# Optimization experiments

Hardware: AMD Instinct MI355X
Metric: run time of the kernel (lower is better)

The kernel has to match this reference:

```python
import jax, jax.numpy as jnp
import numpy as np

V, NLAB, NLAYERS, DI, DM, DS, DD, K = 32000, 9, 2, 768, 1536, 16, 96, 4
B, S = 2, 2048
EPS = 1e-6


def setup_inputs() -> dict:
    key = jax.random.key(0)
    ks = jax.random.split(key, 12)
    n = lambda k, shape, s=0.02: jax.random.normal(k, shape, jnp.float32) * s
    return {
        "input_ids": jax.random.randint(ks[0], (B, S), 0, V, dtype=jnp.int32),
        "attention_mask": jnp.ones((B, S), jnp.int32),
        "emb": n(ks[1], (V, DI)),
        "norm_w": jnp.ones((NLAYERS, DI), jnp.float32),
        "in_proj_w": n(ks[2], (NLAYERS, 2 * DM, DI)),
        "conv_w": n(ks[3], (NLAYERS, DM, K), 0.1),
        "conv_b": jnp.zeros((NLAYERS, DM), jnp.float32),
        "sB_w": n(ks[4], (NLAYERS, DS, DM)),
        "sC_w": n(ks[5], (NLAYERS, DS, DM)),
        "sD1_w": n(ks[6], (NLAYERS, DD, DM)),
        "sD2_w": n(ks[7], (NLAYERS, DM, DD)),
        "A": jnp.tile(jnp.arange(1, DS + 1, dtype=jnp.float32), (NLAYERS, DM, 1)),
        "Dp": jnp.ones((NLAYERS, DM), jnp.float32),
        "out_w": n(ks[8], (NLAYERS, DI, DM)),
        "cls_w": n(ks[9], (NLAB, DI)),
        "cls_b": jnp.zeros((NLAB,), jnp.float32),
    }


def _rmsnorm(x, w):
    return x * jax.lax.rsqrt(jnp.mean(x * x, axis=-1, keepdims=True) + EPS) * w


def _mamba_block(x, norm_w, Wi, cw, cb, WB, WC, W1, W2, A, Dp, Wo):
    # x: (b, l, d_input)
    h = _rmsnorm(x, norm_w)
    a, gate = jnp.split(h @ Wi.T, 2, axis=-1)  # each (b, l, DM)
    # causal depthwise conv1d, kernel K, left-pad K-1 (== Conv1d(pad=K-1)[..., :l])
    L = a.shape[1]
    ap = jnp.pad(a, ((0, 0), (K - 1, 0), (0, 0)))
    conv = cb + sum(ap[:, i:i + L, :] * cw[:, i] for i in range(K))
    a = jax.nn.silu(conv)
    # selective SSM
    Bm = a @ WB.T                                   # (b, l, DS)
    Cm = a @ WC.T                                   # (b, l, DS)
    delta = jax.nn.softplus(Dp + (a @ W1.T) @ W2.T)  # (b, l, DM)
    A_bar = jnp.exp(delta[..., None] * (-A))         # (b, l, DM, DS)
    X_bar = (delta * a)[..., None] * Bm[:, :, None, :]  # (b, l, DM, DS)

    def comb(c1, c2):
        a1, x1 = c1
        a2, x2 = c2
        return a1 * a2, a2 * x1 + x2

    _, hid = jax.lax.associative_scan(comb, (A_bar, X_bar), axis=1)
    y = jnp.einsum('blds,bls->bld', hid, Cm) + Dp * a
    y = y * jax.nn.silu(gate)
    return y @ Wo.T


def _forward(input_ids, attention_mask, emb, norm_w, in_proj_w, conv_w, conv_b,
             sB_w, sC_w, sD1_w, sD2_w, A, Dp, out_w, cls_w, cls_b):
    x = emb[input_ids] * attention_mask[..., None].astype(emb.dtype)
    for i in range(NLAYERS):  # residual Mamba layers
        x = _mamba_block(x, norm_w[i], in_proj_w[i], conv_w[i], conv_b[i],
                         sB_w[i], sC_w[i], sD1_w[i], sD2_w[i], A[i], Dp[i], out_w[i]) + x
    # dropout is identity at inference
    return x @ cls_w.T + cls_b  # logits (b, l, num_labels)


def reference(input_ids, attention_mask, emb, norm_w, in_proj_w, conv_w, conv_b,
              sB_w, sC_w, sD1_w, sD2_w, A, Dp, out_w, cls_w, cls_b):
    return _forward(input_ids, attention_mask, emb, norm_w, in_proj_w, conv_w, conv_b,
                    sB_w, sC_w, sD1_w, sD2_w, A, Dp, out_w, cls_w, cls_b)
```

## Files before the change

kernel.cpp:

```cpp
#include <hip/hip_runtime.h>
#include <hip/hip_bf16.h>
#include <math.h>

#define NLAB 9
#define NL   2
#define DI   768
#define DM   1536
#define DS   16
#define KC   4
#define DD   96
#define BB   2
#define SS   2048
#define TT   (BB*SS)
#define EPSF 1e-6f

#define NCH  64
#define CL   (SS/NCH)

#define NW   128
#define KS   8
#define KSL  (DM/KS)

typedef __attribute__((ext_vector_type(4))) float f32x4;
typedef __attribute__((ext_vector_type(8))) short bf16x8;
typedef __attribute__((ext_vector_type(4))) unsigned short us4;

__device__ __forceinline__ float siluf(float x) { return x / (1.f + __expf(-x)); }
__device__ __forceinline__ float softplusf(float x) { return x > 15.f ? x : log1pf(__expf(x)); }

__device__ __forceinline__ unsigned short f2bf(float f) {
    unsigned u = __float_as_uint(f);
    return (unsigned short)((u + 0x7fffu + ((u >> 16) & 1u)) >> 16);
}

__global__ void f32_to_bf16(const float* __restrict__ src,
                            unsigned short* __restrict__ dst, int n)
{
    int i = (blockIdx.x * 256 + threadIdx.x) * 8;
    if (i >= n) return;
    float4 a = *(const float4*)(src + i);
    float4 b = *(const float4*)(src + i + 4);
    union { unsigned short s[8]; uint4 v; } o;
    o.s[0] = f2bf(a.x); o.s[1] = f2bf(a.y); o.s[2] = f2bf(a.z); o.s[3] = f2bf(a.w);
    o.s[4] = f2bf(b.x); o.s[5] = f2bf(b.y); o.s[6] = f2bf(b.z); o.s[7] = f2bf(b.w);
    *(uint4*)(dst + i) = o.v;
}

__global__ void embed_kernel(const int* __restrict__ ids, const int* __restrict__ mask,
                             const float* __restrict__ emb, float* __restrict__ x)
{
    int t = blockIdx.x;
    int i = threadIdx.x;
    float m = (float)mask[t];
    int id = ids[t];
    float4 v = ((const float4*)(emb + (size_t)id * DI))[i];
    v.x *= m; v.y *= m; v.z *= m; v.w *= m;
    ((float4*)(x + (size_t)t * DI))[i] = v;
}

__global__ void rmsnorm_kernel(const float* __restrict__ x, const float* __restrict__ w,
                               unsigned short* __restrict__ h)
{
    __shared__ float red[4];
    int t = blockIdx.x;
    const float* xr = x + (size_t)t * DI;
    float ss = 0.f;
    for (int i = threadIdx.x; i < DI; i += 256) { float v = xr[i]; ss += v * v; }
    #pragma unroll
    for (int m = 1; m < 64; m <<= 1) ss += __shfl_xor(ss, m, 64);
    if ((threadIdx.x & 63) == 0) red[threadIdx.x >> 6] = ss;
    __syncthreads();
    float scale = rsqrtf((red[0] + red[1] + red[2] + red[3]) * (1.f / DI) + EPSF);
    for (int i = threadIdx.x; i < DI; i += 256)
        h[(size_t)t * DI + i] = f2bf(xr[i] * scale * w[i]);
}

#define STAGE_TILE(AS, BS, KT) do {                                                           \
    _Pragma("unroll")                                                                         \
    for (int it = 0; it < 2; ++it) {                                                          \
        int rbase = it * 64 + wave * 16;                                                      \
        int row = rbase + (lane >> 2);                                                        \
        int c8 = (((lane & 3) ^ ((lane >> 3) & 3)) * 8);                                      \
        __builtin_amdgcn_global_load_lds(                                                     \
            (const __attribute__((address_space(1))) unsigned int*)(Arow + (size_t)row * lda + (KT) + c8), \
            (__attribute__((address_space(3))) unsigned int*)((AS) + rbase * 32), 16, 0, 0);  \
        __builtin_amdgcn_global_load_lds(                                                     \
            (const __attribute__((address_space(1))) unsigned int*)(Brow + (size_t)row * ldb + (KT) + c8), \
            (__attribute__((address_space(3))) unsigned int*)((BS) + rbase * 32), 16, 0, 0);  \
    } } while (0)

#define COMPUTE_TILE(AS, BS) do {                                                             \
    bf16x8 af[4], bfr[4];                                                                     \
    const int khs = (kh ^ ((lr >> 1) & 3)) * 8;                                               \
    _Pragma("unroll")                                                                         \
    for (int i = 0; i < 4; ++i)                                                               \
        af[i] = *(const bf16x8*)&(AS)[(wm + i * 16 + lr) * 32 + khs];                         \
    _Pragma("unroll")                                                                         \
    for (int j = 0; j < 4; ++j)                                                               \
        bfr[j] = *(const bf16x8*)&(BS)[(wn + j * 16 + lr) * 32 + khs];                        \
    _Pragma("unroll")                                                                         \
    for (int i = 0; i < 4; ++i)                                                               \
        _Pragma("unroll")                                                                     \
        for (int j = 0; j < 4; ++j)                                                           \
            acc[i][j] = __builtin_amdgcn_mfma_f32_16x16x32_bf16(af[i], bfr[j], acc[i][j], 0, 0, 0); \
    } while (0)

#define WAIT_BAR(T, NT) do {                                                                  \
    if ((T) + 1 < (NT)) asm volatile("s_waitcnt vmcnt(4)" ::: "memory");                      \
    else                asm volatile("s_waitcnt vmcnt(0)" ::: "memory");                      \
    __builtin_amdgcn_s_barrier();                                                             \
} while (0)

__global__ __launch_bounds__(256) void gemm_bf16(
    const unsigned short* __restrict__ A, const unsigned short* __restrict__ B,
    const float* __restrict__ Rres, const float* __restrict__ bias,
    float* __restrict__ C, int M, int N, int K,
    int lda, int ldb, int ldc, int act, int cstride)
{
    __shared__ unsigned short As0[128 * 32];
    __shared__ unsigned short Bs0[128 * 32];
    __shared__ unsigned short As1[128 * 32];
    __shared__ unsigned short Bs1[128 * 32];
    __shared__ unsigned short As2[128 * 32];
    __shared__ unsigned short Bs2[128 * 32];
    const int tid = threadIdx.x;
    const int wave = tid >> 6, lane = tid & 63;

    const int nwg = gridDim.x * gridDim.y;
    int flat = blockIdx.y * gridDim.x + blockIdx.x;
    int nf = (flat & 7) * (nwg >> 3) + (flat >> 3);
    const int bm = (nf / gridDim.x) * 128;
    const int bn = (nf % gridDim.x) * 128;

    const int wm = (wave >> 1) * 64, wn = (wave & 1) * 64;
    const int lr = lane & 15, kh = lane >> 4;

    f32x4 acc[4][4] = {};

    const unsigned short* Arow = A + (size_t)bm * lda;
    const unsigned short* Brow = B + (size_t)bn * ldb;

    const int nt = K >> 5;
    STAGE_TILE(As0, Bs0, 0);
    if (nt > 1) STAGE_TILE(As1, Bs1, 32);

    int t = 0;
    while (true) {
        WAIT_BAR(t, nt);
        if (t + 2 < nt) STAGE_TILE(As2, Bs2, (t + 2) * 32);
        COMPUTE_TILE(As0, Bs0);
        if (++t == nt) break;
        WAIT_BAR(t, nt);
        if (t + 2 < nt) STAGE_TILE(As0, Bs0, (t + 2) * 32);
        COMPUTE_TILE(As1, Bs1);
        if (++t == nt) break;
        WAIT_BAR(t, nt);
        if (t + 2 < nt) STAGE_TILE(As1, Bs1, (t + 2) * 32);
        COMPUTE_TILE(As2, Bs2);
        if (++t == nt) break;
    }

    #pragma unroll
    for (int i = 0; i < 4; ++i) {
        #pragma unroll
        for (int j = 0; j < 4; ++j) {
            #pragma unroll
            for (int r = 0; r < 4; ++r) {
                int row = bm + wm + i * 16 + kh * 4 + r;
                int col = bn + wn + j * 16 + lr;
                float v = acc[i][j][r];
                if (bias) v += bias[col];
                if (act == 1) v = softplusf(v);
                if (Rres) v += Rres[(size_t)row * ldc + col];
                C[((size_t)row * ldc + col) * cstride] = v;
            }
        }
    }
}

__global__ __launch_bounds__(256) void gemm_skinny_bf16(
    const unsigned short* __restrict__ A, const unsigned short* __restrict__ B,
    float* __restrict__ Part)
{
    __shared__ unsigned short As0[128 * 32];
    __shared__ unsigned short Bs0[128 * 32];
    __shared__ unsigned short As1[128 * 32];
    __shared__ unsigned short Bs1[128 * 32];
    __shared__ unsigned short As2[128 * 32];
    __shared__ unsigned short Bs2[128 * 32];
    const int tid = threadIdx.x;
    const int wave = tid >> 6, lane = tid & 63;
    const int bm = blockIdx.x * 128;
    const int ks = blockIdx.y;
    const int k0 = ks * KSL;
    const int wm = (wave >> 1) * 64, wn = (wave & 1) * 64;
    const int lr = lane & 15, kh = lane >> 4;
    const int lda = DM, ldb = DM;

    f32x4 acc[4][4] = {};

    const unsigned short* Arow = A + (size_t)bm * DM;
    const unsigned short* Brow = B;

    const int nt = KSL >> 5;
    STAGE_TILE(As0, Bs0, k0);
    STAGE_TILE(As1, Bs1, k0 + 32);

    int t = 0;
    while (true) {
        WAIT_BAR(t, nt);
        if (t + 2 < nt) STAGE_TILE(As2, Bs2, k0 + (t + 2) * 32);
        COMPUTE_TILE(As0, Bs0);
        if (++t == nt) break;
        WAIT_BAR(t, nt);
        if (t + 2 < nt) STAGE_TILE(As0, Bs0, k0 + (t + 2) * 32);
        COMPUTE_TILE(As1, Bs1);
        if (++t == nt) break;
        WAIT_BAR(t, nt);
        if (t + 2 < nt) STAGE_TILE(As1, Bs1, k0 + (t + 2) * 32);
        COMPUTE_TILE(As2, Bs2);
        if (++t == nt) break;
    }

    float* out = Part + (size_t)ks * TT * NW;
    #pragma unroll
    for (int i = 0; i < 4; ++i) {
        #pragma unroll
        for (int j = 0; j < 4; ++j) {
            #pragma unroll
            for (int r = 0; r < 4; ++r) {
                int row = bm + wm + i * 16 + kh * 4 + r;
                int col = wn + j * 16 + lr;
                out[(size_t)row * NW + col] = acc[i][j][r];
            }
        }
    }
}

__global__ void skinny_reduce(const float* __restrict__ Part,
                              float* __restrict__ BCD, unsigned short* __restrict__ dd16)
{
    int idx = blockIdx.x * 256 + threadIdx.x;
    float s = 0.f;
    #pragma unroll
    for (int ks = 0; ks < KS; ++ks)
        s += Part[(size_t)ks * TT * NW + idx];
    BCD[idx] = s;
    int col = idx & (NW - 1);
    if (col >= 32)
        dd16[(size_t)(idx >> 7) * DD + (col - 32)] = f2bf(s);
}

__global__ void conv_silu_kernel(const float* __restrict__ proj, const float* __restrict__ cw,
                                 const float* __restrict__ cb, float* __restrict__ av,
                                 unsigned short* __restrict__ aconv16)
{
    int t = blockIdx.x;
    int d = blockIdx.y * 256 + threadIdx.x;
    int p = t & (SS - 1);
    float acc = cb[d];
    #pragma unroll
    for (int j = 0; j < KC; ++j) {
        int pp = p - (KC - 1) + j;
        if (pp >= 0)
            acc += cw[d * KC + j] * proj[(size_t)(t - (KC - 1) + j) * (2 * DM) + d];
    }
    float v = siluf(acc);
    av[(size_t)t * DM + d] = v;
    aconv16[(size_t)t * DM + d] = f2bf(v);
}

__global__ void concat_w_kernel(const float* __restrict__ WB, const float* __restrict__ WC,
                                const float* __restrict__ W1, unsigned short* __restrict__ Wcat16)
{
    int l = blockIdx.y;
    int row = blockIdx.x;
    const float* src;
    if (row < 16)      src = WB + (size_t)l * DS * DM + (size_t)row * DM;
    else if (row < 32) src = WC + (size_t)l * DS * DM + (size_t)(row - 16) * DM;
    else               src = W1 + (size_t)l * DD * DM + (size_t)(row - 32) * DM;
    unsigned short* dst = Wcat16 + ((size_t)l * NW + row) * DM;
    for (int i = threadIdx.x; i < DM / 4; i += 256) {
        float4 v = ((const float4*)src)[i];
        us4 u = { f2bf(v.x), f2bf(v.y), f2bf(v.z), f2bf(v.w) };
        *(us4*)(dst + i * 4) = u;
    }
}

__global__ __launch_bounds__(256) void scan_pass1(
    const float* __restrict__ dtv, const float* __restrict__ av,
    const float* __restrict__ BCD, const float* __restrict__ Amat,
    float2* __restrict__ PQ)
{
    __shared__ float4 sB4[CL][DS / 4];
    int b = blockIdx.z, c = blockIdx.y;
    int d = blockIdx.x * 256 + threadIdx.x;
    size_t rowbase = (size_t)b * SS + (size_t)c * CL;

    for (int i = threadIdx.x; i < CL * DS; i += 256)
        ((float*)sB4)[i] = BCD[(rowbase + (i >> 4)) * NW + (i & 15)];
    __syncthreads();

    float negA[DS], hid[DS];
    #pragma unroll
    for (int s = 0; s < DS; ++s) {
        negA[s] = -Amat[(size_t)d * DS + s];
        hid[s] = 0.f;
    }
    float cum = 0.f;

    const float* pd = dtv + rowbase * DM + d;
    const float* pa = av  + rowbase * DM + d;
    for (int t = 0; t < CL; ++t) {
        float dt = pd[(size_t)t * DM];
        float avv = pa[(size_t)t * DM];
        cum += dt;
        float xv = dt * avv;
        #pragma unroll
        for (int j = 0; j < DS / 4; ++j) {
            float4 bv = sB4[t][j];
            hid[4*j+0] = __expf(dt * negA[4*j+0]) * hid[4*j+0] + xv * bv.x;
            hid[4*j+1] = __expf(dt * negA[4*j+1]) * hid[4*j+1] + xv * bv.y;
            hid[4*j+2] = __expf(dt * negA[4*j+2]) * hid[4*j+2] + xv * bv.z;
            hid[4*j+3] = __expf(dt * negA[4*j+3]) * hid[4*j+3] + xv * bv.w;
        }
    }
    float2* out = PQ + ((size_t)(b * NCH + c) * DM + d) * DS;
    #pragma unroll
    for (int s = 0; s < DS; ++s)
        out[s] = make_float2(__expf(cum * negA[s]), hid[s]);
}

__global__ void scan_carry(float2* __restrict__ PQ)
{
    int idx = blockIdx.x * 256 + threadIdx.x;
    int b = idx / (DM * DS);
    int r = idx - b * (DM * DS);
    float carry = 0.f;
    #pragma unroll 4
    for (int c = 0; c < NCH; ++c) {
        size_t o = (size_t)(b * NCH + c) * (DM * DS) + r;
        float2 pq = PQ[o];
        PQ[o].x = carry;
        carry = pq.x * carry + pq.y;
    }
}

__global__ __launch_bounds__(256) void scan_pass2(
    const float* __restrict__ dtv, const float* __restrict__ av,
    const float* __restrict__ BCD,
    const float* __restrict__ proj, const float* __restrict__ Amat,
    const float* __restrict__ Dp, const float2* __restrict__ PQ,
    unsigned short* __restrict__ y)
{
    __shared__ float4 sB4[CL][DS / 4];
    __shared__ float4 sC4[CL][DS / 4];
    int b = blockIdx.z, c = blockIdx.y;
    int d = blockIdx.x * 256 + threadIdx.x;
    size_t rowbase = (size_t)b * SS + (size_t)c * CL;

    for (int i = threadIdx.x; i < CL * DS; i += 256) {
        size_t row = rowbase + (i >> 4);
        ((float*)sB4)[i] = BCD[row * NW + (i & 15)];
        ((float*)sC4)[i] = BCD[row * NW + 16 + (i & 15)];
    }
    __syncthreads();

    float negA[DS], hid[DS];
    const float2* pin = PQ + ((size_t)(b * NCH + c) * DM + d) * DS;
    #pragma unroll
    for (int s = 0; s < DS; ++s) {
        negA[s] = -Amat[(size_t)d * DS + s];
        hid[s] = pin[s].x;
    }
    float Dpd = Dp[d];

    const float* pd = dtv + rowbase * DM + d;
    const float* pa = av  + rowbase * DM + d;
    const float* gp = proj + rowbase * (2 * DM) + DM + d;
    unsigned short* yp = y + rowbase * DM + d;

    for (int t = 0; t < CL; ++t) {
        float dt = pd[(size_t)t * DM];
        float avv = pa[(size_t)t * DM];
        float g  = gp[(size_t)t * (2 * DM)];
        float xv = dt * avv;
        float acc0 = 0.f, acc1 = 0.f, acc2 = 0.f, acc3 = 0.f;
        #pragma unroll
        for (int j = 0; j < DS / 4; ++j) {
            float4 bv = sB4[t][j];
            float4 cv = sC4[t][j];
            hid[4*j+0] = __expf(dt * negA[4*j+0]) * hid[4*j+0] + xv * bv.x;
            hid[4*j+1] = __expf(dt * negA[4*j+1]) * hid[4*j+1] + xv * bv.y;
            hid[4*j+2] = __expf(dt * negA[4*j+2]) * hid[4*j+2] + xv * bv.z;
            hid[4*j+3] = __expf(dt * negA[4*j+3]) * hid[4*j+3] + xv * bv.w;
            acc0 += hid[4*j+0] * cv.x;
            acc1 += hid[4*j+1] * cv.y;
            acc2 += hid[4*j+2] * cv.z;
            acc3 += hid[4*j+3] * cv.w;
        }
        float contrib = (acc0 + acc1) + (acc2 + acc3);
        yp[(size_t)t * DM] = f2bf((contrib + Dpd * avv) * siluf(g));
    }
}

__global__ void cls_kernel(const float* __restrict__ x, const float* __restrict__ W,
                           const float* __restrict__ bias, float* __restrict__ out)
{
    int t = blockIdx.x;
    int lane = threadIdx.x;
    const float* xr = x + (size_t)t * DI;
    float acc[NLAB];
    #pragma unroll
    for (int n = 0; n < NLAB; ++n) acc[n] = 0.f;
    for (int i = lane; i < DI; i += 64) {
        float xv = xr[i];
        #pragma unroll
        for (int n = 0; n < NLAB; ++n) acc[n] += xv * W[(size_t)n * DI + i];
    }
    #pragma unroll
    for (int n = 0; n < NLAB; ++n)
        #pragma unroll
        for (int m = 1; m < 64; m <<= 1) acc[n] += __shfl_xor(acc[n], m, 64);
    if (lane < NLAB) out[(size_t)t * NLAB + lane] = acc[lane] + bias[lane];
}

extern "C" void kernel_launch(void* const* d_in, const int* in_sizes, int n_in,
                              void* d_out, int out_size, void* d_ws, size_t ws_size,
                              hipStream_t stream)
{
    const int*   ids    = (const int*)d_in[0];
    const int*   mask   = (const int*)d_in[1];
    const float* emb    = (const float*)d_in[2];
    const float* norm_w = (const float*)d_in[3];
    const float* Wi     = (const float*)d_in[4];
    const float* conv_w = (const float*)d_in[5];
    const float* conv_b = (const float*)d_in[6];
    const float* sB_w   = (const float*)d_in[7];
    const float* sC_w   = (const float*)d_in[8];
    const float* sD1_w  = (const float*)d_in[9];
    const float* sD2_w  = (const float*)d_in[10];
    const float* Amat   = (const float*)d_in[11];
    const float* Dp     = (const float*)d_in[12];
    const float* out_w  = (const float*)d_in[13];
    const float* cls_w  = (const float*)d_in[14];
    const float* cls_b  = (const float*)d_in[15];
    float* logits = (float*)d_out;

    float* ws = (float*)d_ws;
    size_t off = 0;
    float* x     = ws + off; off += (size_t)TT * DI;
    float* proj  = ws + off; off += (size_t)TT * 2 * DM;
    float* dtv   = ws + off; off += (size_t)TT * DM;
    float* av    = ws + off; off += (size_t)TT * DM;
    float* BCD   = ws + off; off += (size_t)TT * NW;
    size_t scratch_sz = (size_t)BB * NCH * DM * DS * 2;
    size_t part_sz = (size_t)KS * TT * NW;
    if (part_sz > scratch_sz) scratch_sz = part_sz;
    float* Part  = ws + off;
    float2* PQ   = (float2*)(ws + off); off += scratch_sz;
    unsigned short* y16     = (unsigned short*)(ws + off); off += (size_t)TT * DM / 2;
    unsigned short* aconv16 = (unsigned short*)(ws + off); off += (size_t)TT * DM / 2;
    unsigned short* Wi16    = (unsigned short*)(ws + off); off += (size_t)NL * 2 * DM * DI / 2;
    unsigned short* Wo16    = (unsigned short*)(ws + off); off += (size_t)NL * DI * DM / 2;
    unsigned short* W216    = (unsigned short*)(ws + off); off += (size_t)NL * DM * DD / 2;
    unsigned short* dd16    = (unsigned short*)(ws + off); off += (size_t)TT * DD / 2;
    unsigned short* Wcat16  = (unsigned short*)(ws + off); off += (size_t)NL * NW * DM / 2;
    if (ws_size < off * sizeof(float)) return;

    unsigned short* h16 = (unsigned short*)dtv;

    embed_kernel<<<TT, DI / 4, 0, stream>>>(ids, mask, emb, x);
    concat_w_kernel<<<dim3(NW, NL), 256, 0, stream>>>(sB_w, sC_w, sD1_w, Wcat16);

    f32_to_bf16<<<(NL * 2 * DM * DI / 8 + 255) / 256, 256, 0, stream>>>(Wi, Wi16, NL * 2 * DM * DI);
    f32_to_bf16<<<(NL * DI * DM / 8 + 255) / 256, 256, 0, stream>>>(out_w, Wo16, NL * DI * DM);
    f32_to_bf16<<<(NL * DM * DD / 8 + 255) / 256, 256, 0, stream>>>(sD2_w, W216, NL * DM * DD);

    for (int l = 0; l < NL; ++l) {
        const float* cw_l  = conv_w + (size_t)l * DM * KC;
        const float* cb_l  = conv_b + (size_t)l * DM;
        const float* A_l   = Amat  + (size_t)l * DM * DS;
        const float* Dp_l  = Dp    + (size_t)l * DM;
        const float* nw_l  = norm_w + (size_t)l * DI;
        const unsigned short* Wi16_l  = Wi16  + (size_t)l * 2 * DM * DI;
        const unsigned short* Wo16_l  = Wo16  + (size_t)l * DI * DM;
        const unsigned short* W216_l  = W216  + (size_t)l * DM * DD;
        const unsigned short* Wcat16_l = Wcat16 + (size_t)l * NW * DM;

        rmsnorm_kernel<<<TT, 256, 0, stream>>>(x, nw_l, h16);

        gemm_bf16<<<dim3(2 * DM / 128, TT / 128), 256, 0, stream>>>(
            h16, Wi16_l, nullptr, nullptr, proj, TT, 2 * DM, DI, DI, DI, 2 * DM, 0, 1);

        conv_silu_kernel<<<dim3(TT, DM / 256), 256, 0, stream>>>(proj, cw_l, cb_l, av, aconv16);

        gemm_skinny_bf16<<<dim3(TT / 128, KS), 256, 0, stream>>>(aconv16, Wcat16_l, Part);
        skinny_reduce<<<TT * NW / 256, 256, 0, stream>>>(Part, BCD, dd16);

        gemm_bf16<<<dim3(DM / 128, TT / 128), 256, 0, stream>>>(
            dd16, W216_l, nullptr, Dp_l, dtv, TT, DM, DD, DD, DD, DM, 1, 1);

        scan_pass1<<<dim3(DM / 256, NCH, BB), 256, 0, stream>>>(dtv, av, BCD, A_l, PQ);
        scan_carry<<<BB * DM * DS / 256, 256, 0, stream>>>(PQ);
        scan_pass2<<<dim3(DM / 256, NCH, BB), 256, 0, stream>>>(
            dtv, av, BCD, proj, A_l, Dp_l, PQ, y16);

        gemm_bf16<<<dim3(DI / 128, TT / 128), 256, 0, stream>>>(
            y16, Wo16_l, x, nullptr, x, TT, DI, DM, DM, DM, DI, 0, 1);
    }

    cls_kernel<<<TT, 64, 0, stream>>>(x, cls_w, cls_b, logits);
}
```

Measured before the change: 731.6 us.

## Add 256x256-tile bf16 GEMM for in_proj and XCD-aware block mapping

```diff
diff --git a/kernel.cpp b/kernel.cpp
--- a/kernel.cpp
+++ b/kernel.cpp
@@ -31,6 +31,18 @@
 __device__ __forceinline__ unsigned short f2bf(float f) {
     unsigned u = __float_as_uint(f);
     return (unsigned short)((u + 0x7fffu + ((u >> 16) & 1u)) >> 16);
+}
+
+__device__ __forceinline__ void xcd_map(int gx, int gy, int bx, int by,
+                                        int& bmt, int& bnt)
+{
+    int flat = by * gx + bx;
+    if ((gx & 1) == 0 && (gy & 3) == 0) {
+        int halfx = gx >> 1, quarty = gy >> 2;
+        int xcd = flat & 7, local = flat >> 3;
+        bnt = (xcd & 1) * halfx + local % halfx;
+        bmt = (xcd >> 1) * quarty + local / halfx;
+    } else { bmt = by; bnt = bx; }
 }
 
 __global__ void f32_to_bf16(const float* __restrict__ src,
@@ -126,11 +138,9 @@
     const int tid = threadIdx.x;
     const int wave = tid >> 6, lane = tid & 63;
 
-    const int nwg = gridDim.x * gridDim.y;
-    int flat = blockIdx.y * gridDim.x + blockIdx.x;
-    int nf = (flat & 7) * (nwg >> 3) + (flat >> 3);
-    const int bm = (nf / gridDim.x) * 128;
-    const int bn = (nf % gridDim.x) * 128;
+    int bmt, bnt;
+    xcd_map(gridDim.x, gridDim.y, blockIdx.x, blockIdx.y, bmt, bnt);
+    const int bm = bmt * 128, bn = bnt * 128;
 
     const int wm = (wave >> 1) * 64, wn = (wave & 1) * 64;
     const int lr = lane & 15, kh = lane >> 4;
@@ -173,6 +183,98 @@
                 if (act == 1) v = softplusf(v);
                 if (Rres) v += Rres[(size_t)row * ldc + col];
                 C[((size_t)row * ldc + col) * cstride] = v;
+            }
+        }
+    }
+}
+
+#define STAGE256(AS, BS, KT) do {                                                             \
+    _Pragma("unroll")                                                                         \
+    for (int it = 0; it < 2; ++it) {                                                          \
+        _Pragma("unroll")                                                                     \
+        for (int hf = 0; hf < 2; ++hf) {                                                      \
+            int rbase = it * 128 + wave * 16;                                                 \
+            int row = rbase + (lane >> 2);                                                    \
+            int c8 = (((lane & 3) ^ ((lane >> 3) & 3)) * 8);                                  \
+            __builtin_amdgcn_global_load_lds(                                                 \
+                (const __attribute__((address_space(1))) unsigned int*)(Arow + (size_t)row * lda + (KT) + hf * 32 + c8), \
+                (__attribute__((address_space(3))) unsigned int*)((AS) + hf * 8192 + rbase * 32), 16, 0, 0); \
+            __builtin_amdgcn_global_load_lds(                                                 \
+                (const __attribute__((address_space(1))) unsigned int*)(Brow + (size_t)row * ldb + (KT) + hf * 32 + c8), \
+                (__attribute__((address_space(3))) unsigned int*)((BS) + hf * 8192 + rbase * 32), 16, 0, 0); \
+        } } } while (0)
+
+#define COMPUTE256(AS, BS) do {                                                               \
+    _Pragma("unroll")                                                                         \
+    for (int hf = 0; hf < 2; ++hf) {                                                          \
+        bf16x8 af[8], bfr[4];                                                                 \
+        const int khs = (kh ^ ((lr >> 1) & 3)) * 8;                                           \
+        _Pragma("unroll")                                                                     \
+        for (int i = 0; i < 8; ++i)                                                           \
+            af[i] = *(const bf16x8*)&(AS)[hf * 8192 + (wm + i * 16 + lr) * 32 + khs];         \
+        _Pragma("unroll")                                                                     \
+        for (int j = 0; j < 4; ++j)                                                           \
+            bfr[j] = *(const bf16x8*)&(BS)[hf * 8192 + (wn + j * 16 + lr) * 32 + khs];        \
+        _Pragma("unroll")                                                                     \
+        for (int i = 0; i < 8; ++i)                                                           \
+            _Pragma("unroll")                                                                 \
+            for (int j = 0; j < 4; ++j)                                                       \
+                acc[i][j] = __builtin_amdgcn_mfma_f32_16x16x32_bf16(af[i], bfr[j], acc[i][j], 0, 0, 0); \
+    } } while (0)
+
+__global__ __launch_bounds__(512, 2) void gemm_bf16_256(
+    const unsigned short* __restrict__ A, const unsigned short* __restrict__ B,
+    float* __restrict__ C, int K, int lda, int ldb, int ldc)
+{
+    __shared__ unsigned short As0[16384];
+    __shared__ unsigned short Bs0[16384];
+    __shared__ unsigned short As1[16384];
+    __shared__ unsigned short Bs1[16384];
+    const int tid = threadIdx.x;
+    const int wave = tid >> 6, lane = tid & 63;
+
+    int bmt, bnt;
+    xcd_map(gridDim.x, gridDim.y, blockIdx.x, blockIdx.y, bmt, bnt);
+    const int bm = bmt * 256, bn = bnt * 256;
+
+    const int wm = (wave >> 2) * 128, wn = (wave & 3) * 64;
+    const int lr = lane & 15, kh = lane >> 4;
+
+    f32x4 acc[8][4] = {};
+
+    const unsigned short* Arow = A + (size_t)bm * lda;
+    const unsigned short* Brow = B + (size_t)bn * ldb;
+
+    const int ntk = K >> 6;
+    STAGE256(As0, Bs0, 0);
+
+    int t = 0;
+    while (true) {
+        if (t + 1 < ntk) { STAGE256(As1, Bs1, (t + 1) * 64);
+                           asm volatile("s_waitcnt vmcnt(8)" ::: "memory"); }
+        else             { asm volatile("s_waitcnt vmcnt(0)" ::: "memory"); }
+        __builtin_amdgcn_s_barrier();
+        COMPUTE256(As0, Bs0);
+        __builtin_amdgcn_s_barrier();
+        if (++t == ntk) break;
+        if (t + 1 < ntk) { STAGE256(As0, Bs0, (t + 1) * 64);
+                           asm volatile("s_waitcnt vmcnt(8)" ::: "memory"); }
+        else             { asm volatile("s_waitcnt vmcnt(0)" ::: "memory"); }
+        __builtin_amdgcn_s_barrier();
+        COMPUTE256(As1, Bs1);
+        __builtin_amdgcn_s_barrier();
+        if (++t == ntk) break;
+    }
+
+    #pragma unroll
+    for (int i = 0; i < 8; ++i) {
+        #pragma unroll
+        for (int j = 0; j < 4; ++j) {
+            #pragma unroll
+            for (int r = 0; r < 4; ++r) {
+                int row = bm + wm + i * 16 + kh * 4 + r;
+                int col = bn + wn + j * 16 + lr;
+                C[(size_t)row * ldc + col] = acc[i][j][r];
             }
         }
     }
@@ -490,8 +592,8 @@
 
         rmsnorm_kernel<<<TT, 256, 0, stream>>>(x, nw_l, h16);
 
-        gemm_bf16<<<dim3(2 * DM / 128, TT / 128), 256, 0, stream>>>(
-            h16, Wi16_l, nullptr, nullptr, proj, TT, 2 * DM, DI, DI, DI, 2 * DM, 0, 1);
+        gemm_bf16_256<<<dim3(2 * DM / 256, TT / 256), 512, 0, stream>>>(
+            h16, Wi16_l, proj, DI, DI, DI, 2 * DM);
 
         conv_silu_kernel<<<dim3(TT, DM / 256), 256, 0, stream>>>(proj, cw_l, cb_l, av, aconv16);
 
```

Measured after the change: 760.3 us. 1.04x slower.
